# Optimization experiments

Hardware: AMD Instinct MI355X
Metric: run time of the kernel (lower is better)

## Reference

```python
import jax, jax.numpy as jnp
import numpy as np

IN_F, H, T, NUM_CLASSES, WINDOW_HALF = 14, 24, 25, 4, 12


def _lstm_dir(x_tbf, w_ih, w_hh, b_ih, b_hh, reverse):
    # x_tbf: [T,B,F]; w_ih: [4H,F]; w_hh: [4H,H]; biases: [4H]
    B = x_tbf.shape[1]
    xw = jnp.einsum('tbf,gf->tbg', x_tbf, w_ih) + b_ih + b_hh  # [T,B,4H]

    def step(carry, xw_t):
        h, c = carry
        gates = xw_t + h @ w_hh.T
        i, f, g, o = jnp.split(gates, 4, axis=-1)
        i, f, o = jax.nn.sigmoid(i), jax.nn.sigmoid(f), jax.nn.sigmoid(o)
        g = jnp.tanh(g)
        c = f * c + i * g
        h = o * jnp.tanh(c)
        return (h, c), h

    h0 = jnp.zeros((B, H), x_tbf.dtype)
    c0 = jnp.zeros((B, H), x_tbf.dtype)
    _, hs = jax.lax.scan(step, (h0, c0), xw, reverse=reverse)
    return hs  # [T,B,H], in original time order


def setup_inputs() -> dict:
    key = jax.random.key(0)
    ks = jax.random.split(key, 12)
    s_ih = 1.0 / np.sqrt(H)
    u = lambda k, shape: jax.random.uniform(k, shape, jnp.float32, -s_ih, s_ih)
    return {
        'x': jax.random.normal(ks[0], (65536, T, IN_F), jnp.float32),
        'w_ih_f': u(ks[1], (4 * H, IN_F)),
        'w_hh_f': u(ks[2], (4 * H, H)),
        'b_ih_f': u(ks[3], (4 * H,)),
        'b_hh_f': u(ks[4], (4 * H,)),
        'w_ih_b': u(ks[5], (4 * H, IN_F)),
        'w_hh_b': u(ks[6], (4 * H, H)),
        'b_ih_b': u(ks[7], (4 * H,)),
        'b_hh_b': u(ks[8], (4 * H,)),
        'head_w': u(ks[9], (NUM_CLASSES, 2 * H)),
        'head_b': u(ks[10], (NUM_CLASSES,)),
    }


def reference(x, w_ih_f, w_hh_f, b_ih_f, b_hh_f, w_ih_b, w_hh_b, b_ih_b, b_hh_b, head_w, head_b):
    x_tbf = jnp.transpose(x, (1, 0, 2))  # [T,B,F]
    h_f = _lstm_dir(x_tbf, w_ih_f, w_hh_f, b_ih_f, b_hh_f, reverse=False)
    h_b = _lstm_dir(x_tbf, w_ih_b, w_hh_b, b_ih_b, b_hh_b, reverse=True)
    center = jnp.concatenate([h_f[WINDOW_HALF], h_b[WINDOW_HALF]], axis=-1)  # [B,2H]
    # dropout is identity in eval mode
    return center @ head_w.T + head_b  # [B,4]
```

## Files before the change

kernel.cpp:

```cpp
#include <hip/hip_runtime.h>

typedef __attribute__((ext_vector_type(8))) short frag8;
typedef __attribute__((ext_vector_type(4))) float f4;
typedef __attribute__((ext_vector_type(4))) unsigned int u4;
typedef __attribute__((ext_vector_type(2))) float f2;

namespace {
constexpr int T_STEPS = 25;
constexpr int IN_F    = 14;
constexpr int H       = 24;
constexpr int NSTEP   = 13;
constexpr float LOG2E    = 1.4426950408889634f;
constexpr float TWOLOG2E = 2.8853900817779268f;
}

#if __has_builtin(__builtin_amdgcn_exp2f)
#define EXP2F(v) __builtin_amdgcn_exp2f(v)
#else
#define EXP2F(v) __expf(0.6931471805599453f * (v))
#endif

__device__ __forceinline__ unsigned short bf16_rne(float f) {
    unsigned int u = __float_as_uint(f);
    u += 0x7fff + ((u >> 16) & 1);
    return (unsigned short)(u >> 16);
}
__device__ __forceinline__ float bf16_to_f(unsigned short s) {
    return __uint_as_float(((unsigned int)s) << 16);
}
__device__ __forceinline__ float fast_rcp(float x) { return __builtin_amdgcn_rcpf(x); }

__global__ void pack_mfma(const float* __restrict__ wif, const float* __restrict__ whf,
                          const float* __restrict__ bif, const float* __restrict__ bhf,
                          const float* __restrict__ wib, const float* __restrict__ whb,
                          const float* __restrict__ bib, const float* __restrict__ bhb,
                          unsigned short* __restrict__ ws)
{
    const int gid = blockIdx.x * 256 + threadIdx.x;
    if (gid >= 1536) return;
    const int lane = gid & 63;
    const int tile = (gid >> 6) % 6;
    const int set  = (gid / 384) & 1;
    const int dir  = gid / 768;
    const int m = lane & 15, q = lane >> 4;
    const int g = (tile < 4) ? tile : (m & 3);
    const int u_row = (tile < 4) ? m : ((tile == 4 ? 16 : 20) + (m >> 2));
    const float* Wx = dir ? wib : wif;
    const float* Wh = dir ? whb : whf;
    const float* bi = dir ? bib : bif;
    const float* bh = dir ? bhb : bhf;
    const int rowW = g * 24 + u_row;
    const float scale = (g == 2) ? TWOLOG2E : -LOG2E;
    unsigned short vals[8];
    #pragma unroll
    for (int j = 0; j < 8; ++j) {
        unsigned short o = 0;
        if (set == 0) {
            if (q < 3) {
                const int f = 4 * q + (j & 3);
                o = bf16_rne(scale * Wx[rowW * IN_F + f]);
            } else {
                if (j == 0 || j == 4)      o = bf16_rne(scale * Wx[rowW * IN_F + 12]);
                else if (j == 1 || j == 5) o = bf16_rne(scale * Wx[rowW * IN_F + 13]);
                else if (j == 2 || j == 3) {
                    const float b = scale * (bi[rowW] + bh[rowW]);
                    const unsigned short hi = bf16_rne(b);
                    o = (j == 2) ? hi : bf16_rne(b - bf16_to_f(hi));
                }
            }
        } else {
            const int k = q * 8 + j;
            const int j7 = k & 7, kq = k >> 3;
            int uh = -1;
            if (j7 < 4)       uh = kq * 4 + j7;
            else if (j7 == 4) uh = 16 + kq;
            else if (j7 == 5) uh = 20 + kq;
            if (uh >= 0) o = bf16_rne(scale * Wh[rowW * H + uh]);
        }
        vals[j] = o;
    }
    unsigned short* d = ws + (size_t)gid * 8;
    #pragma unroll
    for (int j = 0; j < 8; ++j) d[j] = vals[j];
}

__device__ __forceinline__ void lstm_gates(const f4* acc, f4& cv, float& c_s0, float& c_s1,
                                           f4& Hv, float& h_s0, float& h_s1,
                                           frag8& Bhh, frag8& Bhl)
{
    f4 EI, EF, EG, EO, EC;
    #pragma unroll
    for (int r = 0; r < 4; ++r) {
        EI[r] = EXP2F(acc[0][r]);
        EF[r] = EXP2F(acc[1][r]);
        EG[r] = EXP2F(acc[2][r]);
        EO[r] = EXP2F(acc[3][r]);
    }
    const f4 P  = (EI + 1.0f) * (EG + 1.0f);
    const f4 Df = P * (EF + 1.0f);
    f4 Rf;
    #pragma unroll
    for (int r = 0; r < 4; ++r) Rf[r] = fast_rcp(Df[r]);
    cv = (cv * P + (EG - 1.0f) * (EF + 1.0f)) * Rf;
    #pragma unroll
    for (int r = 0; r < 4; ++r) EC[r] = EXP2F(TWOLOG2E * cv[r]);
    const f4 Do = (EO + 1.0f) * (EC + 1.0f);
    f4 Ro;
    #pragma unroll
    for (int r = 0; r < 4; ++r) Ro[r] = fast_rcp(Do[r]);
    Hv = (EC - 1.0f) * Ro;

    float hs[2];
    float cs[2] = {c_s0, c_s1};
    #pragma unroll
    for (int s = 0; s < 2; ++s) {
        const float ei = EXP2F(acc[4 + s][0]);
        const float ef = EXP2F(acc[4 + s][1]);
        const float eg = EXP2F(acc[4 + s][2]);
        const float eo = EXP2F(acc[4 + s][3]);
        const float P2 = (1.0f + ei) * (1.0f + eg);
        const float cn = (cs[s] * P2 + (eg - 1.0f) * (1.0f + ef))
                         * fast_rcp(P2 * (1.0f + ef));
        cs[s] = cn;
        const float ec = EXP2F(TWOLOG2E * cn);
        hs[s] = (ec - 1.0f) * fast_rcp((1.0f + eo) * (1.0f + ec));
    }
    c_s0 = cs[0]; c_s1 = cs[1];
    h_s0 = hs[0]; h_s1 = hs[1];

    f4 Hl;
    #pragma unroll
    for (int r = 0; r < 4; ++r)
        Hl[r] = Hv[r] - __uint_as_float(__float_as_uint(Hv[r]) & 0xFFFF0000u);
    const float hl4 = hs[0] - __uint_as_float(__float_as_uint(hs[0]) & 0xFFFF0000u);
    const float hl5 = hs[1] - __uint_as_float(__float_as_uint(hs[1]) & 0xFFFF0000u);
    const u4 uh4 = {
        __builtin_amdgcn_perm(__float_as_uint(Hv[1]), __float_as_uint(Hv[0]), 0x07060302u),
        __builtin_amdgcn_perm(__float_as_uint(Hv[3]), __float_as_uint(Hv[2]), 0x07060302u),
        __builtin_amdgcn_perm(__float_as_uint(hs[1]), __float_as_uint(hs[0]), 0x07060302u),
        0u};
    const u4 ul4 = {
        __builtin_amdgcn_perm(__float_as_uint(Hl[1]), __float_as_uint(Hl[0]), 0x07060302u),
        __builtin_amdgcn_perm(__float_as_uint(Hl[3]), __float_as_uint(Hl[2]), 0x07060302u),
        __builtin_amdgcn_perm(__float_as_uint(hl5), __float_as_uint(hl4), 0x07060302u),
        0u};
    Bhh = __builtin_bit_cast(frag8, uh4);
    Bhl = __builtin_bit_cast(frag8, ul4);
}

__global__ __launch_bounds__(128, 4)
void bilstm_mfma(const float* __restrict__ x, const unsigned short* __restrict__ wpk,
                 const float* __restrict__ head_w, const float* __restrict__ head_b,
                 float* __restrict__ out, int B)
{
    __align__(16) __shared__ unsigned char arena[2 * 1536];

    const int tid  = threadIdx.x;
    const int wave = __builtin_amdgcn_readfirstlane(tid >> 6);
    const int lane = tid & 63;
    const int q    = lane >> 4;
    const int col  = lane & 15;
    const int b0   = blockIdx.x * 16;

    frag8 Aw[2][6];
    #pragma unroll
    for (int s = 0; s < 2; ++s)
        #pragma unroll
        for (int t = 0; t < 6; ++t)
            Aw[s][t] = ((const frag8*)wpk)[((wave * 2 + s) * 6 + t) * 64 + lane];

    const bool q3 = (q == 3);
    const unsigned int biasor = q3 ? 0x3F803F80u : 0u;
    const int  boff  = q3 ? 40 : q * 16;
    const int  t0    = wave ? (T_STEPS - 1) : 0;
    const int  dstep = wave ? -(IN_F * 4) : (IN_F * 4);
    const char* px = (const char*)x
                   + ((size_t)(b0 + col) * T_STEPS + t0) * (IN_F * 4) + boff;

    auto build_bx = [&](f2 la, f2 lb) -> frag8 {
        const float a0 = q3 ? lb.x : la.x;
        const float a1 = q3 ? lb.y : la.y;
        const float a2 = q3 ? 0.0f : lb.x;
        const float a3 = q3 ? 0.0f : lb.y;
        const float l0 = a0 - __uint_as_float(__float_as_uint(a0) & 0xFFFF0000u);
        const float l1 = a1 - __uint_as_float(__float_as_uint(a1) & 0xFFFF0000u);
        const float l2 = a2 - __uint_as_float(__float_as_uint(a2) & 0xFFFF0000u);
        const float l3 = a3 - __uint_as_float(__float_as_uint(a3) & 0xFFFF0000u);
        const u4 w = {
            __builtin_amdgcn_perm(__float_as_uint(a1), __float_as_uint(a0), 0x07060302u),
            __builtin_amdgcn_perm(__float_as_uint(a3), __float_as_uint(a2), 0x07060302u) | biasor,
            __builtin_amdgcn_perm(__float_as_uint(l1), __float_as_uint(l0), 0x07060302u),
            __builtin_amdgcn_perm(__float_as_uint(l3), __float_as_uint(l2), 0x07060302u)};
        return __builtin_bit_cast(frag8, w);
    };

    f4    cv = {0.f, 0.f, 0.f, 0.f};
    float c_s0 = 0.f, c_s1 = 0.f;
    f4    Hv;
    float h_s0, h_s1;
    frag8 Bhh, Bhl;
    const f4 zc = {0.f, 0.f, 0.f, 0.f};

    f2 la = *(const f2*)px;
    f2 lb = *(const f2*)(px + 8);
    px += dstep;

    {
        const frag8 Bx = build_bx(la, lb);
        la = *(const f2*)px; lb = *(const f2*)(px + 8); px += dstep;
        f4 acc[6];
        #pragma unroll
        for (int t = 0; t < 6; ++t)
            acc[t] = __builtin_amdgcn_mfma_f32_16x16x32_bf16(Aw[0][t], Bx, zc, 0, 0, 0);
        lstm_gates(acc, cv, c_s0, c_s1, Hv, h_s0, h_s1, Bhh, Bhl);
    }

    #pragma unroll 1
    for (int s = 1; s < NSTEP; ++s) {
        const frag8 Bx = build_bx(la, lb);
        la = *(const f2*)px; lb = *(const f2*)(px + 8); px += dstep;
        f4 acc[6];
        #pragma unroll
        for (int t = 0; t < 6; ++t) {
            acc[t] = __builtin_amdgcn_mfma_f32_16x16x32_bf16(Aw[0][t], Bx,  zc,     0, 0, 0);
            acc[t] = __builtin_amdgcn_mfma_f32_16x16x32_bf16(Aw[1][t], Bhh, acc[t], 0, 0, 0);
            acc[t] = __builtin_amdgcn_mfma_f32_16x16x32_bf16(Aw[1][t], Bhl, acc[t], 0, 0, 0);
        }
        lstm_gates(acc, cv, c_s0, c_s1, Hv, h_s0, h_s1, Bhh, Bhl);
    }

    unsigned char* hbase = arena + wave * 1536;
    *(f4*)(hbase + col * 96 + q * 16) = Hv;
    *(float*)(hbase + col * 96 + 64 + q * 4) = h_s0;
    *(float*)(hbase + col * 96 + 80 + q * 4) = h_s1;

    __syncthreads();

    if (tid < 64) {
        const int e = tid >> 2, cls = tid & 3;
        float acc = head_b[cls];
        const float* hf = (const float*)(arena + e * 96);
        const float* hb = (const float*)(arena + 1536 + e * 96);
        #pragma unroll
        for (int u = 0; u < H; ++u)
            acc += hf[u] * head_w[cls * 2 * H + u] + hb[u] * head_w[cls * 2 * H + H + u];
        out[(size_t)b0 * 4 + tid] = acc;
    }
}

extern "C" void kernel_launch(void* const* d_in, const int* in_sizes, int n_in,
                              void* d_out, int out_size, void* d_ws, size_t ws_size,
                              hipStream_t stream)
{
    const float* x      = (const float*)d_in[0];
    const float* w_ih_f = (const float*)d_in[1];
    const float* w_hh_f = (const float*)d_in[2];
    const float* b_ih_f = (const float*)d_in[3];
    const float* b_hh_f = (const float*)d_in[4];
    const float* w_ih_b = (const float*)d_in[5];
    const float* w_hh_b = (const float*)d_in[6];
    const float* b_ih_b = (const float*)d_in[7];
    const float* b_hh_b = (const float*)d_in[8];
    const float* head_w = (const float*)d_in[9];
    const float* head_b = (const float*)d_in[10];
    float* out = (float*)d_out;
    unsigned short* ws = (unsigned short*)d_ws;

    const int B = in_sizes[0] / (T_STEPS * IN_F);

    hipLaunchKernelGGL(pack_mfma, dim3(6), dim3(256), 0, stream,
                       w_ih_f, w_hh_f, b_ih_f, b_hh_f,
                       w_ih_b, w_hh_b, b_ih_b, b_hh_b, ws);
    hipLaunchKernelGGL(bilstm_mfma, dim3((B + 15) / 16), dim3(128), 0, stream,
                       x, ws, head_w, head_b, out, B);
}
```

Before: 178.3 us.

## Pack x and recurrent h into one K=32 operand, staging bf16 x in LDS

Repacks the weight fragments so each 32-wide K slice holds both recurrent-hidden weights and input weights plus bias, which cuts the per-step MFMA chain from three instructions to two per gate tile. The input sequence is preloaded once per wave into shared memory as bf16 pairs with a bias-one slot, replacing per-step global loads and hi/lo splitting of x. The cost is that x drops to single bf16 precision (no low-part correction), LDS use rises to about 14 KB per block, which may limit occupancy, and there is a prologue copy phase.

```diff
diff --git a/kernel.cpp b/kernel.cpp
--- a/kernel.cpp
+++ b/kernel.cpp
@@ -3,6 +3,7 @@
 typedef __attribute__((ext_vector_type(8))) short frag8;
 typedef __attribute__((ext_vector_type(4))) float f4;
 typedef __attribute__((ext_vector_type(4))) unsigned int u4;
+typedef __attribute__((ext_vector_type(2))) unsigned int u2;
 typedef __attribute__((ext_vector_type(2))) float f2;
 
 namespace {
@@ -10,6 +11,8 @@
 constexpr int IN_F    = 14;
 constexpr int H       = 24;
 constexpr int NSTEP   = 13;
+constexpr int STEP_B  = 512;
+constexpr int WAVE_REGION = 14 * STEP_B;
 constexpr float LOG2E    = 1.4426950408889634f;
 constexpr float TWOLOG2E = 2.8853900817779268f;
 }
@@ -40,11 +43,11 @@
     if (gid >= 1536) return;
     const int lane = gid & 63;
     const int tile = (gid >> 6) % 6;
-    const int set  = (gid / 384) & 1;
+    const int m    = (gid / 384) & 1;
     const int dir  = gid / 768;
-    const int m = lane & 15, q = lane >> 4;
-    const int g = (tile < 4) ? tile : (m & 3);
-    const int u_row = (tile < 4) ? m : ((tile == 4 ? 16 : 20) + (m >> 2));
+    const int rm = lane & 15, qA = lane >> 4;
+    const int g = (tile < 4) ? tile : (rm & 3);
+    const int u_row = (tile < 4) ? rm : ((tile == 4 ? 16 : 20) + (rm >> 2));
     const float* Wx = dir ? wib : wif;
     const float* Wh = dir ? whb : whf;
     const float* bi = dir ? bib : bif;
@@ -54,28 +57,21 @@
     unsigned short vals[8];
     #pragma unroll
     for (int j = 0; j < 8; ++j) {
-        unsigned short o = 0;
-        if (set == 0) {
-            if (q < 3) {
-                const int f = 4 * q + (j & 3);
-                o = bf16_rne(scale * Wx[rowW * IN_F + f]);
+        unsigned short o;
+        if (j < 6) {
+            const int uh = (j < 4) ? (qA * 4 + j) : ((j == 4 ? 16 : 20) + qA);
+            o = bf16_rne(scale * Wh[rowW * H + uh]);
+        } else {
+            const int jj = j - 6;
+            if (m == 0) {
+                o = bf16_rne(scale * Wx[rowW * IN_F + 4 * qA + jj]);
+            } else if (qA < 3) {
+                o = bf16_rne(scale * Wx[rowW * IN_F + 4 * qA + 2 + jj]);
             } else {
-                if (j == 0 || j == 4)      o = bf16_rne(scale * Wx[rowW * IN_F + 12]);
-                else if (j == 1 || j == 5) o = bf16_rne(scale * Wx[rowW * IN_F + 13]);
-                else if (j == 2 || j == 3) {
-                    const float b = scale * (bi[rowW] + bh[rowW]);
-                    const unsigned short hi = bf16_rne(b);
-                    o = (j == 2) ? hi : bf16_rne(b - bf16_to_f(hi));
-                }
+                const float b = scale * (bi[rowW] + bh[rowW]);
+                const unsigned short hi = bf16_rne(b);
+                o = (jj == 0) ? hi : bf16_rne(b - bf16_to_f(hi));
             }
-        } else {
-            const int k = q * 8 + j;
-            const int j7 = k & 7, kq = k >> 3;
-            int uh = -1;
-            if (j7 < 4)       uh = kq * 4 + j7;
-            else if (j7 == 4) uh = 16 + kq;
-            else if (j7 == 5) uh = 20 + kq;
-            if (uh >= 0) o = bf16_rne(scale * Wh[rowW * H + uh]);
         }
         vals[j] = o;
     }
@@ -86,7 +82,8 @@
 
 __device__ __forceinline__ void lstm_gates(const f4* acc, f4& cv, float& c_s0, float& c_s1,
                                            f4& Hv, float& h_s0, float& h_s1,
-                                           frag8& Bhh, frag8& Bhl)
+                                           unsigned int& uh0, unsigned int& uh1, unsigned int& uh2,
+                                           unsigned int& ul0, unsigned int& ul1, unsigned int& ul2)
 {
     f4 EI, EF, EG, EO, EC;
     #pragma unroll
@@ -134,18 +131,12 @@
         Hl[r] = Hv[r] - __uint_as_float(__float_as_uint(Hv[r]) & 0xFFFF0000u);
     const float hl4 = hs[0] - __uint_as_float(__float_as_uint(hs[0]) & 0xFFFF0000u);
     const float hl5 = hs[1] - __uint_as_float(__float_as_uint(hs[1]) & 0xFFFF0000u);
-    const u4 uh4 = {
-        __builtin_amdgcn_perm(__float_as_uint(Hv[1]), __float_as_uint(Hv[0]), 0x07060302u),
-        __builtin_amdgcn_perm(__float_as_uint(Hv[3]), __float_as_uint(Hv[2]), 0x07060302u),
-        __builtin_amdgcn_perm(__float_as_uint(hs[1]), __float_as_uint(hs[0]), 0x07060302u),
-        0u};
-    const u4 ul4 = {
-        __builtin_amdgcn_perm(__float_as_uint(Hl[1]), __float_as_uint(Hl[0]), 0x07060302u),
-        __builtin_amdgcn_perm(__float_as_uint(Hl[3]), __float_as_uint(Hl[2]), 0x07060302u),
-        __builtin_amdgcn_perm(__float_as_uint(hl5), __float_as_uint(hl4), 0x07060302u),
-        0u};
-    Bhh = __builtin_bit_cast(frag8, uh4);
-    Bhl = __builtin_bit_cast(frag8, ul4);
+    uh0 = __builtin_amdgcn_perm(__float_as_uint(Hv[1]), __float_as_uint(Hv[0]), 0x07060302u);
+    uh1 = __builtin_amdgcn_perm(__float_as_uint(Hv[3]), __float_as_uint(Hv[2]), 0x07060302u);
+    uh2 = __builtin_amdgcn_perm(__float_as_uint(hs[1]), __float_as_uint(hs[0]), 0x07060302u);
+    ul0 = __builtin_amdgcn_perm(__float_as_uint(Hl[1]), __float_as_uint(Hl[0]), 0x07060302u);
+    ul1 = __builtin_amdgcn_perm(__float_as_uint(Hl[3]), __float_as_uint(Hl[2]), 0x07060302u);
+    ul2 = __builtin_amdgcn_perm(__float_as_uint(hl5), __float_as_uint(hl4), 0x07060302u);
 }
 
 __global__ __launch_bounds__(128, 4)
@@ -153,7 +144,7 @@
                  const float* __restrict__ head_w, const float* __restrict__ head_b,
                  float* __restrict__ out, int B)
 {
-    __align__(16) __shared__ unsigned char arena[2 * 1536];
+    __align__(16) __shared__ unsigned char arena[2 * WAVE_REGION];
 
     const int tid  = threadIdx.x;
     const int wave = __builtin_amdgcn_readfirstlane(tid >> 6);
@@ -164,75 +155,59 @@
 
     frag8 Aw[2][6];
     #pragma unroll
-    for (int s = 0; s < 2; ++s)
+    for (int m = 0; m < 2; ++m)
         #pragma unroll
         for (int t = 0; t < 6; ++t)
-            Aw[s][t] = ((const frag8*)wpk)[((wave * 2 + s) * 6 + t) * 64 + lane];
-
-    const bool q3 = (q == 3);
-    const unsigned int biasor = q3 ? 0x3F803F80u : 0u;
-    const int  boff  = q3 ? 40 : q * 16;
-    const int  t0    = wave ? (T_STEPS - 1) : 0;
-    const int  dstep = wave ? -(IN_F * 4) : (IN_F * 4);
-    const char* px = (const char*)x
-                   + ((size_t)(b0 + col) * T_STEPS + t0) * (IN_F * 4) + boff;
-
-    auto build_bx = [&](f2 la, f2 lb) -> frag8 {
-        const float a0 = q3 ? lb.x : la.x;
-        const float a1 = q3 ? lb.y : la.y;
-        const float a2 = q3 ? 0.0f : lb.x;
-        const float a3 = q3 ? 0.0f : lb.y;
-        const float l0 = a0 - __uint_as_float(__float_as_uint(a0) & 0xFFFF0000u);
-        const float l1 = a1 - __uint_as_float(__float_as_uint(a1) & 0xFFFF0000u);
-        const float l2 = a2 - __uint_as_float(__float_as_uint(a2) & 0xFFFF0000u);
-        const float l3 = a3 - __uint_as_float(__float_as_uint(a3) & 0xFFFF0000u);
-        const u4 w = {
-            __builtin_amdgcn_perm(__float_as_uint(a1), __float_as_uint(a0), 0x07060302u),
-            __builtin_amdgcn_perm(__float_as_uint(a3), __float_as_uint(a2), 0x07060302u) | biasor,
-            __builtin_amdgcn_perm(__float_as_uint(l1), __float_as_uint(l0), 0x07060302u),
-            __builtin_amdgcn_perm(__float_as_uint(l3), __float_as_uint(l2), 0x07060302u)};
-        return __builtin_bit_cast(frag8, w);
-    };
+            Aw[m][t] = ((const frag8*)wpk)[((wave * 2 + m) * 6 + t) * 64 + lane];
+
+    unsigned char* xbase = arena + wave * WAVE_REGION;
+
+    for (int tau = lane; tau < NSTEP * 16; tau += 64) {
+        const int t = tau >> 4, e = tau & 15;
+        const int tt = wave ? (T_STEPS - 1 - t) : t;
+        const float* xr = x + ((size_t)(b0 + e) * T_STEPS + tt) * IN_F;
+        f2 p[7];
+        #pragma unroll
+        for (int i = 0; i < 7; ++i) p[i] = *(const f2*)(xr + 2 * i);
+        unsigned int w[7];
+        #pragma unroll
+        for (int i = 0; i < 7; ++i)
+            asm("v_cvt_pk_bf16_f32 %0, %1, %2" : "=v"(w[i]) : "v"(p[i].x), "v"(p[i].y));
+        unsigned char* d = xbase + t * STEP_B + e * 32;
+        *(u4*)d        = (u4){w[0], w[1], w[2], w[3]};
+        *(u4*)(d + 16) = (u4){w[4], w[5], w[6], 0x3F803F80u};
+    }
+
+    const int xoff = col * 32 + q * 8;
 
     f4    cv = {0.f, 0.f, 0.f, 0.f};
     float c_s0 = 0.f, c_s1 = 0.f;
     f4    Hv;
     float h_s0, h_s1;
-    frag8 Bhh, Bhl;
+    unsigned int uh0 = 0, uh1 = 0, uh2 = 0;
+    unsigned int ul0 = 0, ul1 = 0, ul2 = 0;
     const f4 zc = {0.f, 0.f, 0.f, 0.f};
 
-    f2 la = *(const f2*)px;
-    f2 lb = *(const f2*)(px + 8);
-    px += dstep;
-
-    {
-        const frag8 Bx = build_bx(la, lb);
-        la = *(const f2*)px; lb = *(const f2*)(px + 8); px += dstep;
+    u2 xw = *(const u2*)(xbase + xoff);
+
+    #pragma unroll 1
+    for (int s = 0; s < NSTEP; ++s) {
+        const u2 xn = *(const u2*)(xbase + (s + 1) * STEP_B + xoff);
+        const frag8 B0 = __builtin_bit_cast(frag8, (u4){uh0, uh1, uh2, xw.x});
+        const frag8 B1 = __builtin_bit_cast(frag8, (u4){ul0, ul1, ul2, xw.y});
         f4 acc[6];
         #pragma unroll
-        for (int t = 0; t < 6; ++t)
-            acc[t] = __builtin_amdgcn_mfma_f32_16x16x32_bf16(Aw[0][t], Bx, zc, 0, 0, 0);
-        lstm_gates(acc, cv, c_s0, c_s1, Hv, h_s0, h_s1, Bhh, Bhl);
-    }
-
-    #pragma unroll 1
-    for (int s = 1; s < NSTEP; ++s) {
-        const frag8 Bx = build_bx(la, lb);
-        la = *(const f2*)px; lb = *(const f2*)(px + 8); px += dstep;
-        f4 acc[6];
-        #pragma unroll
         for (int t = 0; t < 6; ++t) {
-            acc[t] = __builtin_amdgcn_mfma_f32_16x16x32_bf16(Aw[0][t], Bx,  zc,     0, 0, 0);
-            acc[t] = __builtin_amdgcn_mfma_f32_16x16x32_bf16(Aw[1][t], Bhh, acc[t], 0, 0, 0);
-            acc[t] = __builtin_amdgcn_mfma_f32_16x16x32_bf16(Aw[1][t], Bhl, acc[t], 0, 0, 0);
+            acc[t] = __builtin_amdgcn_mfma_f32_16x16x32_bf16(Aw[0][t], B0, zc,     0, 0, 0);
+            acc[t] = __builtin_amdgcn_mfma_f32_16x16x32_bf16(Aw[1][t], B1, acc[t], 0, 0, 0);
         }
-        lstm_gates(acc, cv, c_s0, c_s1, Hv, h_s0, h_s1, Bhh, Bhl);
-    }
-
-    unsigned char* hbase = arena + wave * 1536;
-    *(f4*)(hbase + col * 96 + q * 16) = Hv;
-    *(float*)(hbase + col * 96 + 64 + q * 4) = h_s0;
-    *(float*)(hbase + col * 96 + 80 + q * 4) = h_s1;
+        lstm_gates(acc, cv, c_s0, c_s1, Hv, h_s0, h_s1, uh0, uh1, uh2, ul0, ul1, ul2);
+        xw = xn;
+    }
+
+    *(f4*)(xbase + col * 96 + q * 16) = Hv;
+    *(float*)(xbase + col * 96 + 64 + q * 4) = h_s0;
+    *(float*)(xbase + col * 96 + 80 + q * 4) = h_s1;
 
     __syncthreads();
 
@@ -240,7 +215,7 @@
         const int e = tid >> 2, cls = tid & 3;
         float acc = head_b[cls];
         const float* hf = (const float*)(arena + e * 96);
-        const float* hb = (const float*)(arena + 1536 + e * 96);
+        const float* hb = (const float*)(arena + WAVE_REGION + e * 96);
         #pragma unroll
         for (int u = 0; u < H; ++u)
             acc += hf[u] * head_w[cls * 2 * H + u] + hb[u] * head_w[cls * 2 * H + H + u];
```

Result: faster. 172.0 us (-3.5%).
